# Optimization experiments

Hardware: AMD Instinct MI355X
Metric: run time of the kernel (lower is better)

Reference implementation:

```python
import jax, jax.numpy as jnp
import numpy as np

N, E, F_IN, F_OUT = 50000, 800000, 256, 64


def setup_inputs() -> dict:
    key = jax.random.key(0)
    k1, k2, k3, k4 = jax.random.split(key, 4)
    x = jax.random.normal(k1, (N, F_IN), dtype=jnp.float32)
    adj = jax.random.randint(k2, (2, E), 0, N, dtype=jnp.int32)
    # GCNConv parameters (glorot-ish init)
    W = jax.random.normal(k3, (F_IN, F_OUT), dtype=jnp.float32) / np.sqrt(F_IN)
    b = jnp.zeros((F_OUT,), dtype=jnp.float32)
    return {"x": x, "adj": adj, "W": W, "b": b}


def reference(x, adj, W, b):
    n = x.shape[0]
    # PyG GCNConv: add self-loops, symmetric normalization D^-1/2 A D^-1/2
    loop = jnp.arange(n, dtype=adj.dtype)
    src = jnp.concatenate([adj[0], loop])  # [E+N]
    dst = jnp.concatenate([adj[1], loop])  # [E+N]
    deg = jax.ops.segment_sum(jnp.ones_like(dst, dtype=x.dtype), dst, num_segments=n)
    dinv = jax.lax.rsqrt(deg)  # deg >= 1 due to self-loops
    norm = dinv[src] * dinv[dst]  # [E+N]
    h = x @ W  # [N, F_OUT] — transform before propagate (GCNConv order)
    msg = h[src] * norm[:, None]  # [E+N, F_OUT]
    out = jax.ops.segment_sum(msg, dst, num_segments=n) + b
    return jax.nn.relu(out)
```

## Files before the change

### kernel.cpp

```cpp
#include <hip/hip_runtime.h>

#define F_IN 256
#define F_OUT 64
#define BSH 7
#define BINW 128
#define NBINS_CAP 512
#define BATCH 4096
#define CSTRIDE 16
#define MAXBIN_CAP 2560

typedef __attribute__((ext_vector_type(8))) short short8;
typedef __attribute__((ext_vector_type(4))) float f32x4;

__device__ inline float bf_lo(unsigned u) { return __uint_as_float(u << 16); }
__device__ inline float bf_hi(unsigned u) { return __uint_as_float(u & 0xFFFF0000u); }
__device__ inline unsigned cvt_pk_bf16(float lo, float hi) {
    unsigned r;
    asm("v_cvt_pk_bf16_f32 %0, %1, %2" : "=v"(r) : "v"(lo), "v"(hi));
    return r;
}
__device__ inline short8 pack_cvt(float4 a, float4 b) {
    union { unsigned u[4]; short8 s; } r;
    r.u[0] = cvt_pk_bf16(a.x, a.y);
    r.u[1] = cvt_pk_bf16(a.z, a.w);
    r.u[2] = cvt_pk_bf16(b.x, b.y);
    r.u[3] = cvt_pk_bf16(b.z, b.w);
    return r.s;
}

__global__ __launch_bounds__(256) void bin_count(const int* __restrict__ adj,
                                                 unsigned* __restrict__ staging,
                                                 int* __restrict__ cursor,
                                                 int E, int nbins, int maxBin) {
    __shared__ int cnt[NBINS_CAP];
    __shared__ int base[NBINS_CAP];
    const int tid = threadIdx.x;
    for (int i = tid; i < NBINS_CAP; i += 256) cnt[i] = 0;
    __syncthreads();

    const int e0 = blockIdx.x * BATCH + tid * 16;
    int S[16], D[16], sl[16];
    int nv = 0;
    if (e0 + 16 <= E) {
#pragma unroll
        for (int k = 0; k < 4; k++) {
            *(int4*)&S[k * 4] = *(const int4*)&adj[e0 + k * 4];
            *(int4*)&D[k * 4] = *(const int4*)&adj[E + e0 + k * 4];
        }
        nv = 16;
    } else if (e0 < E) {
        for (int k = 0; k < 16 && e0 + k < E; k++) {
            S[k] = adj[e0 + k];
            D[k] = adj[E + e0 + k];
            nv++;
        }
    }
#pragma unroll
    for (int j = 0; j < 16; j++) {
        if (j < nv) sl[j] = atomicAdd(&cnt[D[j] >> BSH], 1);
    }
    __syncthreads();
    for (int i = tid; i < nbins; i += 256) {
        int cv = cnt[i];
        base[i] = cv ? atomicAdd(&cursor[i * CSTRIDE], cv) : 0;
    }
    __syncthreads();
#pragma unroll
    for (int j = 0; j < 16; j++) {
        if (j < nv) {
            int b = D[j] >> BSH;
            int pos = base[b] + sl[j];
            if (pos < maxBin)
                staging[(size_t)b * maxBin + pos] =
                    (unsigned)S[j] | ((unsigned)(D[j] & (BINW - 1)) << 16);
        }
    }
}

__global__ __launch_bounds__(512, 4) void gemm_mfma(const float* __restrict__ x,
                                                    const float* __restrict__ W,
                                                    const unsigned* __restrict__ staging,
                                                    const int* __restrict__ cursor,
                                                    unsigned* __restrict__ gu,
                                                    int N, int maxBin) {
    __shared__ unsigned Wf[32 * 64 * 4];
    __shared__ int degL[BINW];
    __shared__ float dinvL[BINW];
    const int b = blockIdx.x;
    const int tid = threadIdx.x;

    if (tid < BINW) degL[tid] = 0;
    for (int p = tid; p < (F_IN / 2) * F_OUT; p += 512) {
        int kp = p >> 6;
        int n = p & 63;
        int k = kp * 2;
        Wf[((k >> 3) * 64 + n) * 4 + ((k & 7) >> 1)] =
            cvt_pk_bf16(W[k * F_OUT + n], W[(k + 1) * F_OUT + n]);
    }
    __syncthreads();

    const int segCnt = min(cursor[b * CSTRIDE], maxBin);
    const unsigned* seg = staging + (size_t)b * maxBin;
    for (int i = tid; i < segCnt; i += 512) atomicAdd(&degL[seg[i] >> 16], 1);
    __syncthreads();
    if (tid < BINW) dinvL[tid] = rsqrtf((float)degL[tid] + 1.0f);
    __syncthreads();

    const int wave = tid >> 6;
    const int lane = tid & 63;
    const int q = lane >> 4;
    const int c = lane & 15;
    const int n0 = b * 128 + wave * 16;
    const int r = min(n0 + c, N - 1);
    const float* p0 = x + (size_t)r * F_IN + q * 8;

    f32x4 acc[4] = {};
#pragma unroll
    for (int s = 0; s < 8; s++) {
        float4 a0 = *(const float4*)(p0 + s * 32);
        float4 a1 = *(const float4*)(p0 + s * 32 + 4);
        short8 ah = pack_cvt(a0, a1);
#pragma unroll
        for (int t = 0; t < 4; t++) {
            short8 bh = *(const short8*)&Wf[((s * 4 + q) * 64 + t * 16 + c) * 4];
            acc[t] = __builtin_amdgcn_mfma_f32_16x16x32_bf16(ah, bh, acc[t], 0, 0, 0);
        }
    }

#pragma unroll
    for (int rr = 0; rr < 4; rr++) {
        int node = n0 + q * 4 + rr;
        float dv = dinvL[wave * 16 + q * 4 + rr];
#pragma unroll
        for (int t = 0; t < 4; t++) {
            float v = acc[t][rr] * dv;
            float o = __shfl_xor(v, 1, 64);
            if (node < N && !(lane & 1)) {
                gu[(size_t)node * 32 + t * 8 + (c >> 1)] = cvt_pk_bf16(v, o);
            }
        }
    }
}

__global__ __launch_bounds__(1024) void gather_bin(const unsigned* __restrict__ staging,
                                                   const int* __restrict__ cursor,
                                                   const unsigned* __restrict__ g32,
                                                   const float* __restrict__ bias,
                                                   float* __restrict__ out,
                                                   int N, int maxBin) {
    __shared__ int cnt[BINW];
    __shared__ int off[BINW];
    __shared__ int wsum[2];
    __shared__ unsigned short binCsr[MAXBIN_CAP];
    const int b = blockIdx.x;
    const int tid = threadIdx.x;
    const int nb0 = b << BSH;

    if (tid < BINW) cnt[tid] = 0;
    __syncthreads();

    const int segCnt = min(cursor[b * CSTRIDE], maxBin);
    const unsigned* seg = staging + (size_t)b * maxBin;

    unsigned ev[3];
    int sl[3];
    int nv = 0;
#pragma unroll
    for (int r = 0; r < 3; r++) {
        int i = tid + r * 1024;
        if (i < segCnt) {
            unsigned e = seg[i];
            ev[r] = e;
            sl[r] = atomicAdd(&cnt[e >> 16], 1);
            nv = r + 1;
        }
    }
    __syncthreads();

    int incl = 0, v = 0;
    if (tid < BINW) {
        v = cnt[tid];
        incl = v;
        const int lane = tid & 63;
        for (int d = 1; d < 64; d <<= 1) {
            int t = __shfl_up(incl, d, 64);
            if (lane >= d) incl += t;
        }
        if (lane == 63) wsum[tid >> 6] = incl;
    }
    __syncthreads();
    if (tid < BINW) off[tid] = incl - v + ((tid >= 64) ? wsum[0] : 0);
    __syncthreads();

#pragma unroll
    for (int r = 0; r < 3; r++) {
        if (r < nv) binCsr[off[ev[r] >> 16] + sl[r]] = (unsigned short)(ev[r] & 0xFFFFu);
    }
    __syncthreads();

    const int wv = tid >> 6;
    const int lane = tid & 63;
    const int grp = lane >> 3;
    const int h = lane & 7;
    const int node = wv * 8 + grp;
    const int gn = nb0 + node;
    const uint4* g4 = (const uint4*)g32;

    if (gn < N) {
        const int start = off[node];
        const int deg = cnt[node];

        float a0[8] = {}, a1[8] = {};
        int i = 0;
        for (; i + 4 <= deg; i += 4) {
            int s0 = binCsr[start + i], s1 = binCsr[start + i + 1];
            int s2 = binCsr[start + i + 2], s3 = binCsr[start + i + 3];
            uint4 u0 = g4[(size_t)s0 * 8 + h];
            uint4 u1 = g4[(size_t)s1 * 8 + h];
            uint4 u2 = g4[(size_t)s2 * 8 + h];
            uint4 u3 = g4[(size_t)s3 * 8 + h];
            a0[0] += bf_lo(u0.x); a0[1] += bf_hi(u0.x);
            a0[2] += bf_lo(u0.y); a0[3] += bf_hi(u0.y);
            a0[4] += bf_lo(u0.z); a0[5] += bf_hi(u0.z);
            a0[6] += bf_lo(u0.w); a0[7] += bf_hi(u0.w);
            a1[0] += bf_lo(u1.x); a1[1] += bf_hi(u1.x);
            a1[2] += bf_lo(u1.y); a1[3] += bf_hi(u1.y);
            a1[4] += bf_lo(u1.z); a1[5] += bf_hi(u1.z);
            a1[6] += bf_lo(u1.w); a1[7] += bf_hi(u1.w);
            a0[0] += bf_lo(u2.x); a0[1] += bf_hi(u2.x);
            a0[2] += bf_lo(u2.y); a0[3] += bf_hi(u2.y);
            a0[4] += bf_lo(u2.z); a0[5] += bf_hi(u2.z);
            a0[6] += bf_lo(u2.w); a0[7] += bf_hi(u2.w);
            a1[0] += bf_lo(u3.x); a1[1] += bf_hi(u3.x);
            a1[2] += bf_lo(u3.y); a1[3] += bf_hi(u3.y);
            a1[4] += bf_lo(u3.z); a1[5] += bf_hi(u3.z);
            a1[6] += bf_lo(u3.w); a1[7] += bf_hi(u3.w);
        }
        for (; i < deg; i++) {
            int s0 = binCsr[start + i];
            uint4 u0 = g4[(size_t)s0 * 8 + h];
            a0[0] += bf_lo(u0.x); a0[1] += bf_hi(u0.x);
            a0[2] += bf_lo(u0.y); a0[3] += bf_hi(u0.y);
            a0[4] += bf_lo(u0.z); a0[5] += bf_hi(u0.z);
            a0[6] += bf_lo(u0.w); a0[7] += bf_hi(u0.w);
        }

        uint4 us = g4[(size_t)gn * 8 + h];
        float dv = rsqrtf((float)deg + 1.0f);
        float s0 = bf_lo(us.x), s1 = bf_hi(us.x), s2 = bf_lo(us.y), s3 = bf_hi(us.y);
        float s4 = bf_lo(us.z), s5 = bf_hi(us.z), s6 = bf_lo(us.w), s7 = bf_hi(us.w);
        float4 b0 = *(const float4*)&bias[h * 8];
        float4 b1 = *(const float4*)&bias[h * 8 + 4];
        float4 r0, r1;
        r0.x = fmaxf(fmaf(dv, a0[0] + a1[0] + s0, b0.x), 0.0f);
        r0.y = fmaxf(fmaf(dv, a0[1] + a1[1] + s1, b0.y), 0.0f);
        r0.z = fmaxf(fmaf(dv, a0[2] + a1[2] + s2, b0.z), 0.0f);
        r0.w = fmaxf(fmaf(dv, a0[3] + a1[3] + s3, b0.w), 0.0f);
        r1.x = fmaxf(fmaf(dv, a0[4] + a1[4] + s4, b1.x), 0.0f);
        r1.y = fmaxf(fmaf(dv, a0[5] + a1[5] + s5, b1.y), 0.0f);
        r1.z = fmaxf(fmaf(dv, a0[6] + a1[6] + s6, b1.z), 0.0f);
        r1.w = fmaxf(fmaf(dv, a0[7] + a1[7] + s7, b1.w), 0.0f);
        *(float4*)&out[(size_t)gn * F_OUT + h * 8] = r0;
        *(float4*)&out[(size_t)gn * F_OUT + h * 8 + 4] = r1;
    }
}

extern "C" void kernel_launch(void* const* d_in, const int* in_sizes, int n_in,
                              void* d_out, int out_size, void* d_ws, size_t ws_size,
                              hipStream_t stream) {
    const float* x = (const float*)d_in[0];
    const int* adj = (const int*)d_in[1];
    const float* W = (const float*)d_in[2];
    const float* b = (const float*)d_in[3];
    float* out = (float*)d_out;

    const int N = in_sizes[0] / F_IN;
    const int E = in_sizes[1] / 2;
    const int nbins = (N + BINW - 1) >> BSH;
    const int maxBin = MAXBIN_CAP;

    char* ws = (char*)d_ws;
    size_t segCur = (((size_t)nbins * CSTRIDE * 4) + 255) & ~(size_t)255;
    size_t segStg = (((size_t)nbins * maxBin * 4) + 255) & ~(size_t)255;
    int* cursor = (int*)ws;
    unsigned* staging = (unsigned*)(ws + segCur);
    unsigned* g16 = (unsigned*)(ws + segCur + segStg);

    hipMemsetAsync(cursor, 0, segCur, stream);

    bin_count<<<(E + BATCH - 1) / BATCH, 256, 0, stream>>>(adj, staging, cursor,
                                                           E, nbins, maxBin);
    gemm_mfma<<<nbins, 512, 0, stream>>>(x, W, staging, cursor, g16, N, maxBin);
    gather_bin<<<nbins, 1024, 0, stream>>>(staging, cursor, g16, b, out, N, maxBin);
}
```

Measured before the change: 133.0 us.

## Fuse edge binning and GEMM into one launch, move degree scaling to new kernel

Edge binning and the x@W GEMM now run as separate block ranges of a single launch, so the two independent stages can overlap on the GPU. The degree normalization that the GEMM used to apply depends on the finished binning, so it moves into a new scale_g kernel. The GEMM now writes an fp32 intermediate h, and scale_g reads it back, scales it by the inverse square-root degree and packs it to bf16. This adds an extra launch and an extra round trip of N×64 floats through global memory in exchange for the overlap.

```diff
diff --git a/kernel.cpp b/kernel.cpp
--- a/kernel.cpp
+++ b/kernel.cpp
@@ -28,82 +28,68 @@
     return r.s;
 }
 
-__global__ __launch_bounds__(256) void bin_count(const int* __restrict__ adj,
-                                                 unsigned* __restrict__ staging,
-                                                 int* __restrict__ cursor,
-                                                 int E, int nbins, int maxBin) {
-    __shared__ int cnt[NBINS_CAP];
-    __shared__ int base[NBINS_CAP];
+__global__ __launch_bounds__(512, 4) void fused_bin_gemm(
+    const float* __restrict__ x, const int* __restrict__ adj,
+    const float* __restrict__ W, unsigned* __restrict__ staging,
+    int* __restrict__ cursor, float* __restrict__ hf32,
+    int N, int E, int nbins, int nbat) {
+    __shared__ union {
+        struct { int cnt[NBINS_CAP]; int base[NBINS_CAP]; } p1;
+        unsigned Wf[32 * 64 * 4];
+    } sh;
     const int tid = threadIdx.x;
-    for (int i = tid; i < NBINS_CAP; i += 256) cnt[i] = 0;
-    __syncthreads();
-
-    const int e0 = blockIdx.x * BATCH + tid * 16;
-    int S[16], D[16], sl[16];
-    int nv = 0;
-    if (e0 + 16 <= E) {
-#pragma unroll
-        for (int k = 0; k < 4; k++) {
-            *(int4*)&S[k * 4] = *(const int4*)&adj[e0 + k * 4];
-            *(int4*)&D[k * 4] = *(const int4*)&adj[E + e0 + k * 4];
-        }
-        nv = 16;
-    } else if (e0 < E) {
-        for (int k = 0; k < 16 && e0 + k < E; k++) {
-            S[k] = adj[e0 + k];
-            D[k] = adj[E + e0 + k];
-            nv++;
-        }
-    }
-#pragma unroll
-    for (int j = 0; j < 16; j++) {
-        if (j < nv) sl[j] = atomicAdd(&cnt[D[j] >> BSH], 1);
-    }
-    __syncthreads();
-    for (int i = tid; i < nbins; i += 256) {
-        int cv = cnt[i];
-        base[i] = cv ? atomicAdd(&cursor[i * CSTRIDE], cv) : 0;
-    }
-    __syncthreads();
-#pragma unroll
-    for (int j = 0; j < 16; j++) {
-        if (j < nv) {
-            int b = D[j] >> BSH;
-            int pos = base[b] + sl[j];
-            if (pos < maxBin)
-                staging[(size_t)b * maxBin + pos] =
-                    (unsigned)S[j] | ((unsigned)(D[j] & (BINW - 1)) << 16);
-        }
-    }
-}
-
-__global__ __launch_bounds__(512, 4) void gemm_mfma(const float* __restrict__ x,
-                                                    const float* __restrict__ W,
-                                                    const unsigned* __restrict__ staging,
-                                                    const int* __restrict__ cursor,
-                                                    unsigned* __restrict__ gu,
-                                                    int N, int maxBin) {
-    __shared__ unsigned Wf[32 * 64 * 4];
-    __shared__ int degL[BINW];
-    __shared__ float dinvL[BINW];
-    const int b = blockIdx.x;
-    const int tid = threadIdx.x;
-
-    if (tid < BINW) degL[tid] = 0;
+
+    if ((int)blockIdx.x < nbat) {
+        for (int i = tid; i < NBINS_CAP; i += 512) sh.p1.cnt[i] = 0;
+        __syncthreads();
+        const int e0 = blockIdx.x * BATCH + tid * 8;
+        int S[8], D[8], sl[8];
+        int nv = 0;
+        if (e0 + 8 <= E) {
+#pragma unroll
+            for (int k = 0; k < 2; k++) {
+                *(int4*)&S[k * 4] = *(const int4*)&adj[e0 + k * 4];
+                *(int4*)&D[k * 4] = *(const int4*)&adj[E + e0 + k * 4];
+            }
+            nv = 8;
+        } else if (e0 < E) {
+            for (int k = 0; k < 8 && e0 + k < E; k++) {
+                S[k] = adj[e0 + k];
+                D[k] = adj[E + e0 + k];
+                nv++;
+            }
+        }
+#pragma unroll
+        for (int j = 0; j < 8; j++) {
+            if (j < nv) sl[j] = atomicAdd(&sh.p1.cnt[D[j] >> BSH], 1);
+        }
+        __syncthreads();
+        for (int i = tid; i < nbins; i += 512) {
+            int cv = sh.p1.cnt[i];
+            sh.p1.base[i] = cv ? atomicAdd(&cursor[i * CSTRIDE], cv) : 0;
+        }
+        __syncthreads();
+#pragma unroll
+        for (int j = 0; j < 8; j++) {
+            if (j < nv) {
+                int b = D[j] >> BSH;
+                int pos = sh.p1.base[b] + sl[j];
+                if (pos < MAXBIN_CAP)
+                    staging[(size_t)b * MAXBIN_CAP + pos] =
+                        (unsigned)S[j] | ((unsigned)(D[j] & (BINW - 1)) << 16);
+            }
+        }
+        return;
+    }
+
+    const int b = blockIdx.x - nbat;
     for (int p = tid; p < (F_IN / 2) * F_OUT; p += 512) {
         int kp = p >> 6;
         int n = p & 63;
         int k = kp * 2;
-        Wf[((k >> 3) * 64 + n) * 4 + ((k & 7) >> 1)] =
+        sh.Wf[((k >> 3) * 64 + n) * 4 + ((k & 7) >> 1)] =
             cvt_pk_bf16(W[k * F_OUT + n], W[(k + 1) * F_OUT + n]);
     }
-    __syncthreads();
-
-    const int segCnt = min(cursor[b * CSTRIDE], maxBin);
-    const unsigned* seg = staging + (size_t)b * maxBin;
-    for (int i = tid; i < segCnt; i += 512) atomicAdd(&degL[seg[i] >> 16], 1);
-    __syncthreads();
-    if (tid < BINW) dinvL[tid] = rsqrtf((float)degL[tid] + 1.0f);
     __syncthreads();
 
     const int wave = tid >> 6;
@@ -122,7 +108,7 @@
         short8 ah = pack_cvt(a0, a1);
 #pragma unroll
         for (int t = 0; t < 4; t++) {
-            short8 bh = *(const short8*)&Wf[((s * 4 + q) * 64 + t * 16 + c) * 4];
+            short8 bh = *(const short8*)&sh.Wf[((s * 4 + q) * 64 + t * 16 + c) * 4];
             acc[t] = __builtin_amdgcn_mfma_f32_16x16x32_bf16(ah, bh, acc[t], 0, 0, 0);
         }
     }
@@ -130,14 +116,44 @@
 #pragma unroll
     for (int rr = 0; rr < 4; rr++) {
         int node = n0 + q * 4 + rr;
-        float dv = dinvL[wave * 16 + q * 4 + rr];
-#pragma unroll
-        for (int t = 0; t < 4; t++) {
-            float v = acc[t][rr] * dv;
-            float o = __shfl_xor(v, 1, 64);
-            if (node < N && !(lane & 1)) {
-                gu[(size_t)node * 32 + t * 8 + (c >> 1)] = cvt_pk_bf16(v, o);
+        if (node < N) {
+#pragma unroll
+            for (int t = 0; t < 4; t++) {
+                hf32[(size_t)node * F_OUT + t * 16 + c] = acc[t][rr];
             }
+        }
+    }
+}
+
+__global__ __launch_bounds__(512) void scale_g(const unsigned* __restrict__ staging,
+                                               const int* __restrict__ cursor,
+                                               const float* __restrict__ hf32,
+                                               unsigned* __restrict__ gu, int N) {
+    __shared__ int degL[BINW];
+    __shared__ float dinvL[BINW];
+    const int b = blockIdx.x;
+    const int tid = threadIdx.x;
+    const int nb0 = b << BSH;
+
+    if (tid < BINW) degL[tid] = 0;
+    __syncthreads();
+
+    const int cs = min(cursor[b * CSTRIDE], MAXBIN_CAP);
+    const unsigned* seg = staging + (size_t)b * MAXBIN_CAP;
+    for (int i = tid; i < cs; i += 512) atomicAdd(&degL[seg[i] >> 16], 1);
+    __syncthreads();
+    if (tid < BINW) dinvL[tid] = rsqrtf((float)degL[tid] + 1.0f);
+    __syncthreads();
+
+    for (int idx = tid; idx < BINW * 32; idx += 512) {
+        int node = idx >> 5;
+        int cpr = idx & 31;
+        int gn = nb0 + node;
+        if (gn < N) {
+            float dv = dinvL[node];
+            float lo = hf32[(size_t)gn * F_OUT + cpr * 2] * dv;
+            float hi = hf32[(size_t)gn * F_OUT + cpr * 2 + 1] * dv;
+            gu[(size_t)gn * 32 + cpr] = cvt_pk_bf16(lo, hi);
         }
     }
 }
@@ -146,8 +162,7 @@
                                                    const int* __restrict__ cursor,
                                                    const unsigned* __restrict__ g32,
                                                    const float* __restrict__ bias,
-                                                   float* __restrict__ out,
-                                                   int N, int maxBin) {
+                                                   float* __restrict__ out, int N) {
     __shared__ int cnt[BINW];
     __shared__ int off[BINW];
     __shared__ int wsum[2];
@@ -159,8 +174,8 @@
     if (tid < BINW) cnt[tid] = 0;
     __syncthreads();
 
-    const int segCnt = min(cursor[b * CSTRIDE], maxBin);
-    const unsigned* seg = staging + (size_t)b * maxBin;
+    const int segCnt = min(cursor[b * CSTRIDE], MAXBIN_CAP);
+    const unsigned* seg = staging + (size_t)b * MAXBIN_CAP;
 
     unsigned ev[3];
     int sl[3];
@@ -277,19 +292,22 @@
     const int N = in_sizes[0] / F_IN;
     const int E = in_sizes[1] / 2;
     const int nbins = (N + BINW - 1) >> BSH;
-    const int maxBin = MAXBIN_CAP;
+    const int nbat = (E + BATCH - 1) / BATCH;
+    const int ngemm = nbins;
 
     char* ws = (char*)d_ws;
     size_t segCur = (((size_t)nbins * CSTRIDE * 4) + 255) & ~(size_t)255;
-    size_t segStg = (((size_t)nbins * maxBin * 4) + 255) & ~(size_t)255;
+    size_t segStg = (((size_t)nbins * MAXBIN_CAP * 4) + 255) & ~(size_t)255;
+    size_t segH = (((size_t)N * F_OUT * 4) + 255) & ~(size_t)255;
     int* cursor = (int*)ws;
     unsigned* staging = (unsigned*)(ws + segCur);
-    unsigned* g16 = (unsigned*)(ws + segCur + segStg);
+    float* hf32 = (float*)(ws + segCur + segStg);
+    unsigned* g16 = (unsigned*)(ws + segCur + segStg + segH);
 
     hipMemsetAsync(cursor, 0, segCur, stream);
 
-    bin_count<<<(E + BATCH - 1) / BATCH, 256, 0, stream>>>(adj, staging, cursor,
-                                                           E, nbins, maxBin);
-    gemm_mfma<<<nbins, 512, 0, stream>>>(x, W, staging, cursor, g16, N, maxBin);
-    gather_bin<<<nbins, 1024, 0, stream>>>(staging, cursor, g16, b, out, N, maxBin);
-}
+    fused_bin_gemm<<<nbat + ngemm, 512, 0, stream>>>(x, adj, W, staging, cursor,
+                                                     hf32, N, E, nbins, nbat);
+    scale_g<<<nbins, 512, 0, stream>>>(staging, cursor, hf32, g16, N);
+    gather_bin<<<nbins, 1024, 0, stream>>>(staging, cursor, g16, b, out, N);
+}
```

Result: no change. 131.5 us (-1.1%).
